# Kernel tuning notes

Hardware: AMD Instinct MI355X
Metric: run time of the kernel (lower is better)

The kernel has to match this reference:

```python
import jax, jax.numpy as jnp
import numpy as np

B, F_IN, T, N = 2, 32, 8, 20000
E = 320000
HID, F_OUT = 64, 32


def setup_inputs() -> dict:
    key = jax.random.key(0)
    ks = jax.random.split(key, 8)
    x = jax.random.normal(ks[0], (B, F_IN, T, N), dtype=jnp.float32)
    edge_index = jax.random.randint(ks[1], (2, E), 0, N, dtype=jnp.int64)
    edge_weight = jax.random.uniform(ks[2], (E,), dtype=jnp.float32)
    # GCNConv params (glorot weights, zero bias)
    s1 = float(np.sqrt(6.0 / (F_IN + HID)))
    s2 = float(np.sqrt(6.0 / (HID + F_OUT)))
    W1 = jax.random.uniform(ks[3], (F_IN, HID), minval=-s1, maxval=s1, dtype=jnp.float32)
    b1 = jnp.zeros((HID,), jnp.float32)
    W2 = jax.random.uniform(ks[4], (HID, F_OUT), minval=-s2, maxval=s2, dtype=jnp.float32)
    b2 = jnp.zeros((F_OUT,), jnp.float32)
    return {"x": x, "edge_index": edge_index, "edge_weight": edge_weight,
            "W1": W1, "b1": b1, "W2": W2, "b2": b2}


def reference(x, edge_index, edge_weight, W1, b1, W2, b2):
    Bb, Fin, Tt, Nn = x.shape
    row, col = edge_index[0], edge_index[1]
    # gcn_norm with self loops (fill value 1.0)
    loop = jnp.arange(Nn)
    row_f = jnp.concatenate([row, loop])
    col_f = jnp.concatenate([col, loop])
    ew_f = jnp.concatenate([edge_weight, jnp.ones((Nn,), x.dtype)])
    deg = jnp.zeros((Nn,), x.dtype).at[col_f].add(ew_f)
    deg_inv_sqrt = jnp.where(deg > 0, 1.0 / jnp.sqrt(jnp.where(deg > 0, deg, 1.0)), 0.0)
    norm = deg_inv_sqrt[row_f] * ew_f * deg_inv_sqrt[col_f]  # [E+N]

    # fold (batch, time) together: every time step uses the same graph
    h = x.transpose(0, 2, 3, 1).reshape(Bb * Tt, Nn, Fin)  # [BT, N, F]

    def gcn_conv(h, W, b):
        h = h @ W                                   # linear first (as in GCNConv)
        msg = h[:, row_f, :] * norm[None, :, None]  # gather + weight  [BT, E+N, C]
        agg = jnp.zeros_like(h).at[:, col_f, :].add(msg)  # scatter-add over targets
        return agg + b

    h = gcn_conv(h, W1, b1)      # dropout(p=0.1) is identity in eval mode
    h = jnp.tanh(gcn_conv(h, W2, b2))
    # back to [B, out_channels, T, N]
    return h.reshape(Bb, Tt, Nn, -1).transpose(0, 3, 1, 2)
```

## Files before the change

### kernel.cpp

```cpp
#include <hip/hip_runtime.h>
#include <hip/hip_bf16.h>
#include <hip/hip_fp16.h>

#define NB    2
#define FIN   32
#define TT    8
#define NN    20000
#define BT    16
#define CC    32
#define ROW   512
#define ELLK  64
#define FIX   16777216.0f
#define FIXI  5.9604644775390625e-08f

typedef unsigned int nvec4 __attribute__((ext_vector_type(4)));

__device__ inline float h16tof(unsigned int hi) {
    union { unsigned short u; __half h; } cv;
    cv.u = (unsigned short)hi;
    return __half2float(cv.h);
}

__global__ __launch_bounds__(256) void prep_kernel(const float* __restrict__ x,
                                                   __half* __restrict__ xt,
                                                   const int* __restrict__ ei,
                                                   const float* __restrict__ ew,
                                                   unsigned long long* __restrict__ degcnt,
                                                   unsigned int* __restrict__ ell,
                                                   const float* __restrict__ W1,
                                                   const float* __restrict__ W2,
                                                   const float* __restrict__ b1,
                                                   float* __restrict__ W12T,
                                                   float* __restrict__ bb,
                                                   int N, int E, int gtr, int ge) {
    __shared__ float tile[128][33];
    int bid = blockIdx.x;
    if (bid < gtr) {
        int bt = bid & 15;
        int b = bt >> 3, t = bt & 7;
        int n0 = (bid >> 4) * 128;
#pragma unroll
        for (int it = 0; it < 4; ++it) {
            int idx = it * 256 + threadIdx.x;
            int f = idx >> 5;
            int nq = idx & 31;
            int n = n0 + nq * 4;
            float4 v = make_float4(0.f, 0.f, 0.f, 0.f);
            if (n < N) v = *(const float4*)(x + (size_t)(b * 256 + f * 8 + t) * N + n);
            tile[nq * 4 + 0][f] = v.x;
            tile[nq * 4 + 1][f] = v.y;
            tile[nq * 4 + 2][f] = v.z;
            tile[nq * 4 + 3][f] = v.w;
        }
        __syncthreads();
#pragma unroll
        for (int it = 0; it < 2; ++it) {
            int idx = it * 256 + threadIdx.x;
            int nl = idx >> 2, f0 = idx & 3;
            int n = n0 + nl;
            if (n < N) {
                union { nvec4 u; __half2 h[4]; } o;
#pragma unroll
                for (int k = 0; k < 4; ++k)
                    o.h[k] = __floats2half2_rn(tile[nl][f0 * 8 + k * 2],
                                               tile[nl][f0 * 8 + k * 2 + 1]);
                *(nvec4*)(xt + (size_t)n * ROW + bt * 32 + f0 * 8) = o.u;
            }
        }
    } else if (bid < gtr + ge) {
        int e = (bid - gtr) * 256 + threadIdx.x;
        if (e < E) {
            int r = ei[e], c = ei[E + e];
            float wf = ew[e];
            unsigned int fx = (unsigned int)(wf * FIX + 0.5f);
            unsigned long long old =
                atomicAdd(&degcnt[c], 0x100000000ULL | (unsigned long long)fx);
            unsigned int p = (unsigned int)(old >> 32);
            if (p < ELLK) {
                union { __half h; unsigned short u; } cv;
                cv.h = __float2half_rn(wf);
                ell[(size_t)c * ELLK + p] = ((unsigned int)cv.u << 16) | (unsigned int)r;
            }
        }
    } else {
        for (int i = threadIdx.x; i < 1024; i += 256) {
            int f = i >> 5, c = i & 31;
            float acc = 0.f;
            for (int k = 0; k < 64; ++k) acc += W1[f * 64 + k] * W2[k * 32 + c];
            W12T[c * 32 + f] = acc;
            if (f == 0) {
                float a2 = 0.f;
                for (int k = 0; k < 64; ++k) a2 += b1[k] * W2[k * 32 + c];
                bb[c] = a2;
            }
        }
    }
}

__device__ inline void unpack8n(const nvec4& u, float* f) {
    union { unsigned int v; __half2 h; } c;
    float2 a;
    c.v = u.x; a = __half22float2(c.h); f[0] = a.x; f[1] = a.y;
    c.v = u.y; a = __half22float2(c.h); f[2] = a.x; f[3] = a.y;
    c.v = u.z; a = __half22float2(c.h); f[4] = a.x; f[5] = a.y;
    c.v = u.w; a = __half22float2(c.h); f[6] = a.x; f[7] = a.y;
}

template <bool PASS1>
__global__ __launch_bounds__(256) void agg16_kernel(const __half* __restrict__ src,
                                                    __half* __restrict__ dst,
                                                    const unsigned int* __restrict__ dcl,
                                                    const unsigned int* __restrict__ ell,
                                                    float* __restrict__ rowsum,
                                                    int N) {
    int n = (blockIdx.x * 256 + threadIdx.x) >> 6;
    if (n >= N) return;
    int lane = threadIdx.x & 63;
    int cnt = (int)dcl[2 * n + 1];
    if (cnt > ELLK) cnt = ELLK;
    float dn = (float)dcl[2 * n] * FIXI + 1.0f;
    float dc = rsqrtf(dn);
    float sw = 1.0f / dn;
    const unsigned int* row = ell + (size_t)n * ELLK;
    float acc[8];
    {
        nvec4 u = *(const nvec4*)(src + (size_t)n * ROW + lane * 8);
        float f[8]; unpack8n(u, f);
#pragma unroll
        for (int j = 0; j < 8; ++j) acc[j] = sw * f[j];
    }
    float sumw = 0.f;
    int e = 0;
    for (; e + 8 <= cnt; e += 8) {
        unsigned int raw[8];
#pragma unroll
        for (int j = 0; j < 8; ++j)
            raw[j] = __builtin_nontemporal_load(row + e + j);
        nvec4 u[8];
        float dg[8];
#pragma unroll
        for (int j = 0; j < 8; ++j) {
            unsigned int sn = raw[j] & 0xffffu;
            u[j] = *(const nvec4*)(src + (size_t)sn * ROW + lane * 8);
            dg[j] = (float)dcl[2 * sn];
        }
#pragma unroll
        for (int j = 0; j < 8; ++j) {
            float w = rsqrtf(dg[j] * FIXI + 1.0f) * h16tof(raw[j] >> 16) * dc;
            if (PASS1) sumw += w;
            float f[8]; unpack8n(u[j], f);
#pragma unroll
            for (int q = 0; q < 8; ++q) acc[q] += w * f[q];
        }
    }
    for (; e + 2 <= cnt; e += 2) {
        unsigned int rA = __builtin_nontemporal_load(row + e);
        unsigned int rB = __builtin_nontemporal_load(row + e + 1);
        unsigned int sA = rA & 0xffffu, sB = rB & 0xffffu;
        nvec4 uA = *(const nvec4*)(src + (size_t)sA * ROW + lane * 8);
        nvec4 uB = *(const nvec4*)(src + (size_t)sB * ROW + lane * 8);
        float dgA = (float)dcl[2 * sA], dgB = (float)dcl[2 * sB];
        float fA[8], fB[8]; unpack8n(uA, fA); unpack8n(uB, fB);
        float wA = rsqrtf(dgA * FIXI + 1.0f) * h16tof(rA >> 16) * dc;
        float wB = rsqrtf(dgB * FIXI + 1.0f) * h16tof(rB >> 16) * dc;
        if (PASS1) sumw += wA + wB;
#pragma unroll
        for (int q = 0; q < 8; ++q) acc[q] += wA * fA[q];
#pragma unroll
        for (int q = 0; q < 8; ++q) acc[q] += wB * fB[q];
    }
    if (e < cnt) {
        unsigned int r = __builtin_nontemporal_load(row + e);
        unsigned int sn = r & 0xffffu;
        nvec4 u = *(const nvec4*)(src + (size_t)sn * ROW + lane * 8);
        float w = rsqrtf((float)dcl[2 * sn] * FIXI + 1.0f) * h16tof(r >> 16) * dc;
        float f[8]; unpack8n(u, f);
        if (PASS1) sumw += w;
#pragma unroll
        for (int q = 0; q < 8; ++q) acc[q] += w * f[q];
    }
    if (PASS1 && lane == 0) rowsum[n] = sw + sumw;
    union { nvec4 u; __half2 h[4]; } o;
    o.h[0] = __floats2half2_rn(acc[0], acc[1]);
    o.h[1] = __floats2half2_rn(acc[2], acc[3]);
    o.h[2] = __floats2half2_rn(acc[4], acc[5]);
    o.h[3] = __floats2half2_rn(acc[6], acc[7]);
    __builtin_nontemporal_store(o.u, (nvec4*)(dst + (size_t)n * ROW + lane * 8));
}

__global__ __launch_bounds__(256) void final_kernel(const __half* __restrict__ Z,
                                                    const float* __restrict__ W12T,
                                                    const float* __restrict__ bb,
                                                    const float* __restrict__ b2,
                                                    const float* __restrict__ rowsum,
                                                    float* __restrict__ out, int N) {
    __shared__ float zt[64][36];
    __shared__ float wT[32][36];
    __shared__ float bbs[32], b2s[32], rs[64];
    int bt = blockIdx.y;
    int b = bt >> 3, t = bt & 7;
    int n0 = blockIdx.x * 64;
    int tid = threadIdx.x;
    for (int i = tid; i < 1024; i += 256) wT[i >> 5][i & 31] = W12T[i];
    if (tid < 32) { bbs[tid] = bb[tid]; b2s[tid] = b2[tid]; }
    if (tid < 64) { int n = n0 + tid; rs[tid] = (n < N) ? rowsum[n] : 0.f; }
    for (int i = tid; i < 1024; i += 256) {
        int nl = i >> 4, f2 = i & 15;
        int n = n0 + nl;
        float2 v = make_float2(0.f, 0.f);
        if (n < N) {
            __half2 h = *(const __half2*)(Z + (size_t)n * ROW + bt * 32 + f2 * 2);
            v = __half22float2(h);
        }
        zt[nl][f2 * 2] = v.x;
        zt[nl][f2 * 2 + 1] = v.y;
    }
    __syncthreads();
    int c = tid & 31;
    int g = tid >> 5;
    float w[32];
#pragma unroll
    for (int k = 0; k < 8; ++k) {
        float4 v = *(const float4*)&wT[c][k * 4];
        w[k * 4 + 0] = v.x; w[k * 4 + 1] = v.y; w[k * 4 + 2] = v.z; w[k * 4 + 3] = v.w;
    }
    float cb2 = b2s[c], cbb = bbs[c];
    float res[8];
#pragma unroll
    for (int i = 0; i < 8; ++i) {
        int nl = g * 8 + i;
        float acc = cb2 + rs[nl] * cbb;
#pragma unroll
        for (int k = 0; k < 8; ++k) {
            float4 z4 = *(const float4*)&zt[nl][k * 4];
            acc = fmaf(z4.x, w[k * 4 + 0], acc);
            acc = fmaf(z4.y, w[k * 4 + 1], acc);
            acc = fmaf(z4.z, w[k * 4 + 2], acc);
            acc = fmaf(z4.w, w[k * 4 + 3], acc);
        }
        res[i] = tanhf(acc);
    }
    __syncthreads();
#pragma unroll
    for (int i = 0; i < 8; ++i) {
        int nl = g * 8 + i;
        zt[nl][(c + nl) & 31] = res[i];
    }
    __syncthreads();
    for (int i = tid; i < 2048; i += 256) {
        int cc = i >> 6, nl = i & 63;
        int n = n0 + nl;
        if (n < N) out[(((size_t)b * 32 + cc) * TT + t) * (size_t)NN + n] = zt[nl][(cc + nl) & 31];
    }
}

extern "C" void kernel_launch(void* const* d_in, const int* in_sizes, int n_in,
                              void* d_out, int out_size, void* d_ws, size_t ws_size,
                              hipStream_t stream) {
    const float* x  = (const float*)d_in[0];
    const int*   ei = (const int*)d_in[1];
    const float* ew = (const float*)d_in[2];
    const float* W1 = (const float*)d_in[3];
    const float* b1 = (const float*)d_in[4];
    const float* W2 = (const float*)d_in[5];
    const float* b2 = (const float*)d_in[6];
    float* out = (float*)d_out;

    const int N = NN;
    const int E = in_sizes[2];

    char* p = (char*)d_ws;
    __half* xt = (__half*)p;  p += (size_t)N * ROW * 2;
    __half* Y  = (__half*)p;  p += (size_t)N * ROW * 2;
    __half* Z  = (__half*)p;  p += (size_t)N * ROW * 2;
    unsigned int* ell = (unsigned int*)p; p += (size_t)N * ELLK * 4;
    unsigned long long* degcnt = (unsigned long long*)p; p += (size_t)N * 8;
    float* rowsum  = (float*)p;  p += (size_t)N * 4;
    float* W12T    = (float*)p;  p += 1024 * 4;
    float* bb      = (float*)p;

    (void)hipMemsetAsync(degcnt, 0, (size_t)N * 8, stream);

    int ge  = (E + 255) / 256;
    int gtr = ((N + 127) / 128) * BT;
    prep_kernel<<<gtr + ge + 1, 256, 0, stream>>>(x, xt, ei, ew, degcnt, ell,
                                                  W1, W2, b1, W12T, bb, N, E, gtr, ge);

    const unsigned int* dcl = (const unsigned int*)degcnt;
    int gagg = (N * 64 + 255) / 256;
    agg16_kernel<true ><<<gagg, 256, 0, stream>>>(xt, Y, dcl, ell, rowsum, N);
    agg16_kernel<false><<<gagg, 256, 0, stream>>>(Y, Z, dcl, ell, rowsum, N);

    dim3 gfin((N + 63) / 64, BT);
    final_kernel<<<gfin, 256, 0, stream>>>(Z, W12T, bb, b2, rowsum, out, N);
}
```

Baseline: 163.2 us.

## Cache normalized edge weights in ELL during pass one for reuse in pass two

During the first aggregation pass, lane 0 of each wavefront writes the fully normalized edge weight (as fp16) back into the ELL entry. The second pass reads that weight directly and skips the per-neighbor degree gather and rsqrt. The prep kernel also has each thread handle two edges instead of one and loads x with nontemporal loads. In exchange, pass one does extra global writes, and the normalized weight is rounded to fp16 before it is applied in pass two.

```diff
diff --git a/kernel.cpp b/kernel.cpp
--- a/kernel.cpp
+++ b/kernel.cpp
@@ -19,6 +19,11 @@
     union { unsigned short u; __half h; } cv;
     cv.u = (unsigned short)hi;
     return __half2float(cv.h);
+}
+__device__ inline unsigned int ftoh16(float w) {
+    union { __half h; unsigned short u; } cv;
+    cv.h = __float2half_rn(w);
+    return (unsigned int)cv.u;
 }
 
 __global__ __launch_bounds__(256) void prep_kernel(const float* __restrict__ x,
@@ -32,7 +37,7 @@
                                                    const float* __restrict__ b1,
                                                    float* __restrict__ W12T,
                                                    float* __restrict__ bb,
-                                                   int N, int E, int gtr, int ge) {
+                                                   int N, int E, int gtr, int gep) {
     __shared__ float tile[128][33];
     int bid = blockIdx.x;
     if (bid < gtr) {
@@ -45,12 +50,13 @@
             int f = idx >> 5;
             int nq = idx & 31;
             int n = n0 + nq * 4;
-            float4 v = make_float4(0.f, 0.f, 0.f, 0.f);
-            if (n < N) v = *(const float4*)(x + (size_t)(b * 256 + f * 8 + t) * N + n);
-            tile[nq * 4 + 0][f] = v.x;
-            tile[nq * 4 + 1][f] = v.y;
-            tile[nq * 4 + 2][f] = v.z;
-            tile[nq * 4 + 3][f] = v.w;
+            nvec4 v = {0u, 0u, 0u, 0u};
+            if (n < N) v = __builtin_nontemporal_load(
+                              (const nvec4*)(x + (size_t)(b * 256 + f * 8 + t) * N + n));
+            tile[nq * 4 + 0][f] = __uint_as_float(v.x);
+            tile[nq * 4 + 1][f] = __uint_as_float(v.y);
+            tile[nq * 4 + 2][f] = __uint_as_float(v.z);
+            tile[nq * 4 + 3][f] = __uint_as_float(v.w);
         }
         __syncthreads();
 #pragma unroll
@@ -67,20 +73,29 @@
                 *(nvec4*)(xt + (size_t)n * ROW + bt * 32 + f0 * 8) = o.u;
             }
         }
-    } else if (bid < gtr + ge) {
-        int e = (bid - gtr) * 256 + threadIdx.x;
-        if (e < E) {
-            int r = ei[e], c = ei[E + e];
-            float wf = ew[e];
-            unsigned int fx = (unsigned int)(wf * FIX + 0.5f);
+    } else if (bid < gtr + gep) {
+        int e0 = (bid - gtr) * 512 + threadIdx.x;
+        int e1 = e0 + 256;
+        bool v0 = (e0 < E), v1 = (e1 < E);
+        int r0 = 0, c0 = 0, r1 = 0, c1 = 0;
+        float w0 = 0.f, w1 = 0.f;
+        if (v0) { r0 = ei[e0]; c0 = ei[E + e0]; w0 = ew[e0]; }
+        if (v1) { r1 = ei[e1]; c1 = ei[E + e1]; w1 = ew[e1]; }
+        if (v0) {
+            unsigned int fx = (unsigned int)(w0 * FIX + 0.5f);
             unsigned long long old =
-                atomicAdd(&degcnt[c], 0x100000000ULL | (unsigned long long)fx);
+                atomicAdd(&degcnt[c0], 0x100000000ULL | (unsigned long long)fx);
             unsigned int p = (unsigned int)(old >> 32);
-            if (p < ELLK) {
-                union { __half h; unsigned short u; } cv;
-                cv.h = __float2half_rn(wf);
-                ell[(size_t)c * ELLK + p] = ((unsigned int)cv.u << 16) | (unsigned int)r;
-            }
+            if (p < ELLK)
+                ell[(size_t)c0 * ELLK + p] = (ftoh16(w0) << 16) | (unsigned int)r0;
+        }
+        if (v1) {
+            unsigned int fx = (unsigned int)(w1 * FIX + 0.5f);
+            unsigned long long old =
+                atomicAdd(&degcnt[c1], 0x100000000ULL | (unsigned long long)fx);
+            unsigned int p = (unsigned int)(old >> 32);
+            if (p < ELLK)
+                ell[(size_t)c1 * ELLK + p] = (ftoh16(w1) << 16) | (unsigned int)r1;
         }
     } else {
         for (int i = threadIdx.x; i < 1024; i += 256) {
@@ -110,7 +125,7 @@
 __global__ __launch_bounds__(256) void agg16_kernel(const __half* __restrict__ src,
                                                     __half* __restrict__ dst,
                                                     const unsigned int* __restrict__ dcl,
-                                                    const unsigned int* __restrict__ ell,
+                                                    unsigned int* __restrict__ ell,
                                                     float* __restrict__ rowsum,
                                                     int N) {
     int n = (blockIdx.x * 256 + threadIdx.x) >> 6;
@@ -121,7 +136,7 @@
     float dn = (float)dcl[2 * n] * FIXI + 1.0f;
     float dc = rsqrtf(dn);
     float sw = 1.0f / dn;
-    const unsigned int* row = ell + (size_t)n * ELLK;
+    unsigned int* row = ell + (size_t)n * ELLK;
     float acc[8];
     {
         nvec4 u = *(const nvec4*)(src + (size_t)n * ROW + lane * 8);
@@ -137,33 +152,51 @@
         for (int j = 0; j < 8; ++j)
             raw[j] = __builtin_nontemporal_load(row + e + j);
         nvec4 u[8];
-        float dg[8];
+#pragma unroll
+        for (int j = 0; j < 8; ++j)
+            u[j] = *(const nvec4*)(src + (size_t)(raw[j] & 0xffffu) * ROW + lane * 8);
+        unsigned int nw[8];
 #pragma unroll
         for (int j = 0; j < 8; ++j) {
-            unsigned int sn = raw[j] & 0xffffu;
-            u[j] = *(const nvec4*)(src + (size_t)sn * ROW + lane * 8);
-            dg[j] = (float)dcl[2 * sn];
-        }
-#pragma unroll
-        for (int j = 0; j < 8; ++j) {
-            float w = rsqrtf(dg[j] * FIXI + 1.0f) * h16tof(raw[j] >> 16) * dc;
-            if (PASS1) sumw += w;
+            float w;
+            if (PASS1) {
+                float dg = (float)dcl[2 * (raw[j] & 0xffffu)];
+                w = rsqrtf(dg * FIXI + 1.0f) * h16tof(raw[j] >> 16) * dc;
+                sumw += w;
+                nw[j] = (ftoh16(w) << 16) | (raw[j] & 0xffffu);
+            } else {
+                w = h16tof(raw[j] >> 16);
+            }
             float f[8]; unpack8n(u[j], f);
 #pragma unroll
             for (int q = 0; q < 8; ++q) acc[q] += w * f[q];
+        }
+        if (PASS1 && lane == 0) {
+            nvec4 a = {nw[0], nw[1], nw[2], nw[3]};
+            nvec4 b = {nw[4], nw[5], nw[6], nw[7]};
+            *(nvec4*)(row + e) = a;
+            *(nvec4*)(row + e + 4) = b;
         }
     }
     for (; e + 2 <= cnt; e += 2) {
         unsigned int rA = __builtin_nontemporal_load(row + e);
         unsigned int rB = __builtin_nontemporal_load(row + e + 1);
-        unsigned int sA = rA & 0xffffu, sB = rB & 0xffffu;
-        nvec4 uA = *(const nvec4*)(src + (size_t)sA * ROW + lane * 8);
-        nvec4 uB = *(const nvec4*)(src + (size_t)sB * ROW + lane * 8);
-        float dgA = (float)dcl[2 * sA], dgB = (float)dcl[2 * sB];
+        nvec4 uA = *(const nvec4*)(src + (size_t)(rA & 0xffffu) * ROW + lane * 8);
+        nvec4 uB = *(const nvec4*)(src + (size_t)(rB & 0xffffu) * ROW + lane * 8);
         float fA[8], fB[8]; unpack8n(uA, fA); unpack8n(uB, fB);
-        float wA = rsqrtf(dgA * FIXI + 1.0f) * h16tof(rA >> 16) * dc;
-        float wB = rsqrtf(dgB * FIXI + 1.0f) * h16tof(rB >> 16) * dc;
-        if (PASS1) sumw += wA + wB;
+        float wA, wB;
+        if (PASS1) {
+            wA = rsqrtf((float)dcl[2 * (rA & 0xffffu)] * FIXI + 1.0f) * h16tof(rA >> 16) * dc;
+            wB = rsqrtf((float)dcl[2 * (rB & 0xffffu)] * FIXI + 1.0f) * h16tof(rB >> 16) * dc;
+            sumw += wA + wB;
+            if (lane == 0) {
+                row[e]     = (ftoh16(wA) << 16) | (rA & 0xffffu);
+                row[e + 1] = (ftoh16(wB) << 16) | (rB & 0xffffu);
+            }
+        } else {
+            wA = h16tof(rA >> 16);
+            wB = h16tof(rB >> 16);
+        }
 #pragma unroll
         for (int q = 0; q < 8; ++q) acc[q] += wA * fA[q];
 #pragma unroll
@@ -171,11 +204,16 @@
     }
     if (e < cnt) {
         unsigned int r = __builtin_nontemporal_load(row + e);
-        unsigned int sn = r & 0xffffu;
-        nvec4 u = *(const nvec4*)(src + (size_t)sn * ROW + lane * 8);
-        float w = rsqrtf((float)dcl[2 * sn] * FIXI + 1.0f) * h16tof(r >> 16) * dc;
+        nvec4 u = *(const nvec4*)(src + (size_t)(r & 0xffffu) * ROW + lane * 8);
+        float w;
+        if (PASS1) {
+            w = rsqrtf((float)dcl[2 * (r & 0xffffu)] * FIXI + 1.0f) * h16tof(r >> 16) * dc;
+            sumw += w;
+            if (lane == 0) row[e] = (ftoh16(w) << 16) | (r & 0xffffu);
+        } else {
+            w = h16tof(r >> 16);
+        }
         float f[8]; unpack8n(u, f);
-        if (PASS1) sumw += w;
 #pragma unroll
         for (int q = 0; q < 8; ++q) acc[q] += w * f[q];
     }
@@ -281,10 +319,10 @@
 
     (void)hipMemsetAsync(degcnt, 0, (size_t)N * 8, stream);
 
-    int ge  = (E + 255) / 256;
+    int gep = (E + 511) / 512;
     int gtr = ((N + 127) / 128) * BT;
-    prep_kernel<<<gtr + ge + 1, 256, 0, stream>>>(x, xt, ei, ew, degcnt, ell,
-                                                  W1, W2, b1, W12T, bb, N, E, gtr, ge);
+    prep_kernel<<<gtr + gep + 1, 256, 0, stream>>>(x, xt, ei, ew, degcnt, ell,
+                                                   W1, W2, b1, W12T, bb, N, E, gtr, gep);
 
     const unsigned int* dcl = (const unsigned int*)degcnt;
     int gagg = (N * 64 + 255) / 256;
```

New measurement: 174.1 us. +6.7%, slower.
